# Optimization experiments

Hardware: AMD Instinct MI355X
Metric: run time of the kernel (lower is better)

Reference implementation:

```python
import jax, jax.numpy as jnp
import numpy as np

N = 1_000_000   # total atoms in batched graph
G = 50_000      # number of molecules (graphs)
F = 128         # gnn_out_feats (node feature dim)
H = 128         # classifier_hidden_feats
T = 12          # n_tasks
EPS = 1e-5      # BatchNorm1d eps


def setup_inputs() -> dict:
    key = jax.random.key(0)
    ks = jax.random.split(key, 20)
    s = 0.05
    inp = {}
    inp["node_feats"] = jax.random.normal(ks[0], (N, F), jnp.float32)
    inp["segment_ids"] = jnp.sort(jax.random.randint(ks[1], (N,), 0, G))
    inp["num_graphs"] = G
    # per-task atom weighting: Linear(F,1) per task, stacked -> [T,F]
    inp["atom_w"] = jax.random.normal(ks[2], (T, F), jnp.float32) * s
    inp["atom_b"] = jnp.zeros((T,), jnp.float32)
    # fc_layer 1: Linear(F,H) -> ReLU -> BatchNorm1d(H) (eval mode)
    inp["W1"] = jax.random.normal(ks[3], (T, F, H), jnp.float32) * s
    inp["b1"] = jnp.zeros((T, H), jnp.float32)
    inp["g1"] = jnp.ones((T, H), jnp.float32)
    inp["be1"] = jnp.zeros((T, H), jnp.float32)
    inp["rm1"] = jnp.zeros((T, H), jnp.float32)
    inp["rv1"] = jnp.ones((T, H), jnp.float32)
    # fc_layer 2 and 3: Linear(H,H) -> ReLU -> BatchNorm1d(H)
    inp["W2"] = jax.random.normal(ks[4], (T, H, H), jnp.float32) * s
    inp["b2"] = jnp.zeros((T, H), jnp.float32)
    inp["g2"] = jnp.ones((T, H), jnp.float32)
    inp["be2"] = jnp.zeros((T, H), jnp.float32)
    inp["rm2"] = jnp.zeros((T, H), jnp.float32)
    inp["rv2"] = jnp.ones((T, H), jnp.float32)
    inp["W3"] = jax.random.normal(ks[5], (T, H, H), jnp.float32) * s
    inp["b3"] = jnp.zeros((T, H), jnp.float32)
    inp["g3"] = jnp.ones((T, H), jnp.float32)
    inp["be3"] = jnp.zeros((T, H), jnp.float32)
    inp["rm3"] = jnp.zeros((T, H), jnp.float32)
    inp["rv3"] = jnp.ones((T, H), jnp.float32)
    # output_layer: Linear(H,H) -> ReLU -> Linear(H,1)
    inp["oW1"] = jax.random.normal(ks[6], (T, H, H), jnp.float32) * s
    inp["ob1"] = jnp.zeros((T, H), jnp.float32)
    inp["oW2"] = jax.random.normal(ks[7], (T, H), jnp.float32) * s
    inp["ob2"] = jnp.zeros((T,), jnp.float32)
    return inp


def _fc(x, W, b, g, be, rm, rv):
    # Linear -> ReLU -> BatchNorm1d (eval, running stats), batched over tasks t
    y = jax.nn.relu(jnp.einsum('gti,tio->gto', x, W) + b)
    return (y - rm) * (g * jax.lax.rsqrt(rv + EPS)) + be


def reference(node_feats, segment_ids, num_graphs, atom_w, atom_b,
              W1, b1, g1, be1, rm1, rv1,
              W2, b2, g2, be2, rm2, rv2,
              W3, b3, g3, be3, rm3, rv3,
              oW1, ob1, oW2, ob2):
    n_tasks = atom_w.shape[0]
    # WeightAndSum: per-task sigmoid node weights [N,T]
    w = jax.nn.sigmoid(node_feats @ atom_w.T + atom_b)
    # per-task weighted segment-sum pooling: loop over small fixed task count
    sums = [jax.ops.segment_sum(node_feats * w[:, t:t + 1], segment_ids,
                                num_segments=num_graphs)
            for t in range(n_tasks)]
    mol = jnp.stack(sums, axis=1)  # [G, T, F]
    h = _fc(mol, W1, b1, g1, be1, rm1, rv1)
    h = _fc(h, W2, b2, g2, be2, rm2, rv2)
    h = _fc(h, W3, b3, g3, be3, rm3, rv3)
    z = jax.nn.relu(jnp.einsum('gth,tho->gto', h, oW1) + ob1)
    pred = jnp.einsum('gth,th->gt', z, oW2) + ob2  # [G, T]
    return pred
```

## Files before the change

kernel.cpp:

```cpp
#include <hip/hip_runtime.h>
#include <hip/hip_bf16.h>
#include <hip/hip_fp16.h>

typedef _Float16 f16;
typedef _Float16 f16x2 __attribute__((ext_vector_type(2)));
typedef _Float16 f16x4 __attribute__((ext_vector_type(4)));
typedef _Float16 f16x8 __attribute__((ext_vector_type(8)));
typedef float f32x4 __attribute__((ext_vector_type(4)));

#define BN_EPS 1e-5f

__global__ void seg_starts_k(const int* __restrict__ seg, int N, int G, int* __restrict__ start) {
    int n = blockIdx.x * blockDim.x + threadIdx.x;
    if (n >= N) return;
    int s = seg[n];
    int p = (n == 0) ? -1 : seg[n - 1];
    for (int g = p + 1; g <= s; ++g) start[g] = n;
    if (n == N - 1) {
        for (int g = s + 1; g <= G; ++g) start[g] = N;
    }
}

__global__ void prep_k(const float* __restrict__ W1, const float* __restrict__ b1,
                       const float* __restrict__ W2, const float* __restrict__ b2,
                       const float* __restrict__ W3, const float* __restrict__ b3,
                       const float* __restrict__ oW1, const float* __restrict__ ob1,
                       const float* __restrict__ g1, const float* __restrict__ be1,
                       const float* __restrict__ rm1, const float* __restrict__ rv1,
                       const float* __restrict__ g2, const float* __restrict__ be2,
                       const float* __restrict__ rm2, const float* __restrict__ rv2,
                       const float* __restrict__ g3, const float* __restrict__ be3,
                       const float* __restrict__ rm3, const float* __restrict__ rv3,
                       f16* __restrict__ Wt, float* __restrict__ bp) {
    int T = gridDim.x;
    int t = blockIdx.x, l = blockIdx.y;
    int o = threadIdx.x;
    __shared__ float s_sh[128], c_sh[128];

    const float *W, *b, *gg = nullptr, *be = nullptr, *rm = nullptr, *rv = nullptr;
    if (l == 0)      { W = W1;  b = b1; }
    else if (l == 1) { W = W2;  b = b2;  gg = g1; be = be1; rm = rm1; rv = rv1; }
    else if (l == 2) { W = W3;  b = b3;  gg = g2; be = be2; rm = rm2; rv = rv2; }
    else             { W = oW1; b = ob1; gg = g3; be = be3; rm = rm3; rv = rv3; }

    float s = 1.f, c = 0.f;
    if (gg) {
        float sv = gg[t * 128 + o] * rsqrtf(rv[t * 128 + o] + BN_EPS);
        s = sv;
        c = be[t * 128 + o] - rm[t * 128 + o] * sv;
    }
    s_sh[o] = s;
    c_sh[o] = c;
    __syncthreads();

    const float* Wsrc = W + (size_t)t * 128 * 128;
    f16* Wdst = Wt + (((size_t)l * T + t) * 128 + o) * 128;
    float acc = b[t * 128 + o];
    for (int i = 0; i < 128; ++i) {
        float wv = Wsrc[i * 128 + o];
        Wdst[i] = (f16)(s_sh[i] * wv);
        acc += c_sh[i] * wv;
    }
    bp[((size_t)l * T + t) * 128 + o] = acc;
}

__global__ __launch_bounds__(256) void pool_k(const float* __restrict__ feats,
                                              const float* __restrict__ atom_w,
                                              const float* __restrict__ atom_b,
                                              const int* __restrict__ start,
                                              f16* __restrict__ mol, int G) {
    __shared__ f16 xs_all[4][16][128];
    __shared__ float ws_all[4][16][16];

    int wave = threadIdx.x >> 6;
    int lane = threadIdx.x & 63;
    f16 (*xs)[128] = xs_all[wave];
    float (*wsh)[16] = ws_all[wave];

    int g = blockIdx.x * 4 + wave;
    if (g >= G) return;

    int tcol = lane & 15;
    int kg = lane >> 4;

    f16x8 bfr[4];
    float ab = 0.f;
#pragma unroll
    for (int ks = 0; ks < 4; ++ks) {
        f16x8 v = {};
        if (tcol < 12) {
            const float* s = atom_w + tcol * 128 + ks * 32 + kg * 8;
#pragma unroll
            for (int j = 0; j < 8; ++j) v[j] = (f16)s[j];
        }
        bfr[ks] = v;
    }
    if (tcol < 12) ab = atom_b[tcol];

    float accx[12], accy[12];
#pragma unroll
    for (int t = 0; t < 12; ++t) { accx[t] = 0.f; accy[t] = 0.f; }

    int a0 = start[g], a1 = start[g + 1];

    for (int c0 = a0; c0 < a1; c0 += 16) {
        int cn = a1 - c0; if (cn > 16) cn = 16;
        asm volatile("s_waitcnt lgkmcnt(0)" ::: "memory");
        __builtin_amdgcn_sched_barrier(0);

#pragma unroll
        for (int it = 0; it < 8; ++it) {
            int c = (it << 6) + lane;
            int r = c >> 5, q = c & 31;
            float4 u = make_float4(0.f, 0.f, 0.f, 0.f);
            if (r < cn) u = *(const float4*)(feats + (size_t)(c0 + r) * 128 + (q << 2));
            f16x4 h;
            h[0] = (f16)u.x; h[1] = (f16)u.y; h[2] = (f16)u.z; h[3] = (f16)u.w;
            *(f16x4*)(&xs[r][(((q >> 1) ^ (r & 7)) << 3) + ((q & 1) << 2)]) = h;
        }
        asm volatile("s_waitcnt lgkmcnt(0)" ::: "memory");
        __builtin_amdgcn_sched_barrier(0);

        f32x4 pa = {0.f, 0.f, 0.f, 0.f};
#pragma unroll
        for (int ks = 0; ks < 4; ++ks) {
            f16x8 afr = *(const f16x8*)(&xs[tcol][((((ks << 2) + kg)) ^ (tcol & 7)) << 3]);
            pa = __builtin_amdgcn_mfma_f32_16x16x32_f16(afr, bfr[ks], pa, 0, 0, 0);
        }
#pragma unroll
        for (int j = 0; j < 4; ++j) {
            float w = 1.f / (1.f + __expf(-(pa[j] + ab)));
            wsh[(kg << 2) + j][tcol] = w;
        }
        asm volatile("s_waitcnt lgkmcnt(0)" ::: "memory");
        __builtin_amdgcn_sched_barrier(0);

        for (int a = 0; a < cn; ++a) {
            f16x2 x2 = *(const f16x2*)(&xs[a][(((lane >> 2) ^ (a & 7)) << 3) + ((lane & 3) << 1)]);
            float x0 = (float)x2[0], x1 = (float)x2[1];
            f32x4 w0 = *(const f32x4*)(&wsh[a][0]);
            f32x4 w1 = *(const f32x4*)(&wsh[a][4]);
            f32x4 w2 = *(const f32x4*)(&wsh[a][8]);
#pragma unroll
            for (int j = 0; j < 4; ++j) {
                accx[j] += w0[j] * x0;     accy[j] += w0[j] * x1;
                accx[4 + j] += w1[j] * x0; accy[4 + j] += w1[j] * x1;
                accx[8 + j] += w2[j] * x0; accy[8 + j] += w2[j] * x1;
            }
        }
    }

#pragma unroll
    for (int t = 0; t < 12; ++t) {
        f16x2 h;
        h[0] = (f16)accx[t];
        h[1] = (f16)accy[t];
        *(f16x2*)(mol + ((size_t)t * G + g) * 128 + 2 * lane) = h;
    }
}

__global__ __launch_bounds__(256, 2) void fc_k(const f16* __restrict__ mol,
                                               const f16* __restrict__ Wt,
                                               const float* __restrict__ bp,
                                               const float* __restrict__ oW2,
                                               const float* __restrict__ ob2,
                                               float* __restrict__ out, int G, int T) {
    __shared__ f16 A[2][64][128];
    __shared__ f16 B[128][128];

    int t = blockIdx.y;
    int g0 = blockIdx.x * 64;
    int tid = threadIdx.x;

    {
        const f16* src = mol + (size_t)t * G * 128;
#pragma unroll
        for (int k = 0; k < 4; ++k) {
            int c = tid + k * 256;
            int r = c >> 4, sl = c & 15;
            uint4 v = make_uint4(0u, 0u, 0u, 0u);
            if (g0 + r < G) v = *(const uint4*)(src + (size_t)(g0 + r) * 128 + sl * 8);
            *(uint4*)(&A[0][r][(sl ^ (r & 7)) * 8]) = v;
        }
    }
    {
        const f16* src = Wt + ((size_t)0 * T + t) * 128 * 128;
#pragma unroll
        for (int k = 0; k < 8; ++k) {
            int c = tid + k * 256;
            int r = c >> 4, sl = c & 15;
            uint4 v = *(const uint4*)(src + (size_t)r * 128 + sl * 8);
            *(uint4*)(&B[r][(sl ^ (r & 7)) * 8]) = v;
        }
    }
    __syncthreads();

    int wid = tid >> 6, lane = tid & 63;
    int lg = lane >> 4, lr = lane & 15;
    int m0 = wid * 16;
    int arow = m0 + lr;
    float pred[4] = {0.f, 0.f, 0.f, 0.f};
    int cur = 0;

    for (int l = 0; l < 4; ++l) {
        f16x8 afr[4];
#pragma unroll
        for (int ks = 0; ks < 4; ++ks) {
            int sl = (4 * ks + lg) ^ (arow & 7);
            afr[ks] = *(const f16x8*)(&A[cur][arow][sl * 8]);
        }
        const float* bias = bp + ((size_t)l * T + t) * 128;
#pragma unroll
        for (int nf = 0; nf < 8; ++nf) {
            int n = nf * 16 + lr;
            f32x4 acc = {0.f, 0.f, 0.f, 0.f};
#pragma unroll
            for (int ks = 0; ks < 4; ++ks) {
                int sl = (4 * ks + lg) ^ (n & 7);
                f16x8 bfr = *(const f16x8*)(&B[n][sl * 8]);
                acc = __builtin_amdgcn_mfma_f32_16x16x32_f16(afr[ks], bfr, acc, 0, 0, 0);
            }
            float bv = bias[n];
            if (l < 3) {
#pragma unroll
                for (int j = 0; j < 4; ++j) {
                    float y = acc[j] + bv;
                    y = y > 0.f ? y : 0.f;
                    int rr = m0 + 4 * lg + j;
                    A[cur ^ 1][rr][(((n >> 3) ^ (rr & 7)) << 3) + (n & 7)] = (f16)y;
                }
            } else {
                float w2 = oW2[t * 128 + n];
#pragma unroll
                for (int j = 0; j < 4; ++j) {
                    float z = acc[j] + bv;
                    z = z > 0.f ? z : 0.f;
                    pred[j] += z * w2;
                }
            }
        }
        __syncthreads();
        if (l < 3) {
            const f16* src = Wt + ((size_t)(l + 1) * T + t) * 128 * 128;
#pragma unroll
            for (int k = 0; k < 8; ++k) {
                int c = tid + k * 256;
                int r = c >> 4, sl = c & 15;
                uint4 v = *(const uint4*)(src + (size_t)r * 128 + sl * 8);
                *(uint4*)(&B[r][(sl ^ (r & 7)) * 8]) = v;
            }
            __syncthreads();
            cur ^= 1;
        }
    }

#pragma unroll
    for (int m = 1; m < 16; m <<= 1) {
#pragma unroll
        for (int j = 0; j < 4; ++j) pred[j] += __shfl_xor(pred[j], m, 64);
    }
    if (lr == 0) {
        float ob = ob2[t];
#pragma unroll
        for (int j = 0; j < 4; ++j) {
            int gg = g0 + m0 + 4 * lg + j;
            if (gg < G) out[(size_t)gg * T + t] = pred[j] + ob;
        }
    }
}

extern "C" void kernel_launch(void* const* d_in, const int* in_sizes, int n_in,
                              void* d_out, int out_size, void* d_ws, size_t ws_size,
                              hipStream_t stream) {
    const float* node_feats = (const float*)d_in[0];
    const int*   seg        = (const int*)d_in[1];
    const float* atom_w     = (const float*)d_in[3];
    const float* atom_b     = (const float*)d_in[4];
    const float* W1  = (const float*)d_in[5];
    const float* b1  = (const float*)d_in[6];
    const float* g1  = (const float*)d_in[7];
    const float* be1 = (const float*)d_in[8];
    const float* rm1 = (const float*)d_in[9];
    const float* rv1 = (const float*)d_in[10];
    const float* W2  = (const float*)d_in[11];
    const float* b2  = (const float*)d_in[12];
    const float* g2  = (const float*)d_in[13];
    const float* be2 = (const float*)d_in[14];
    const float* rm2 = (const float*)d_in[15];
    const float* rv2 = (const float*)d_in[16];
    const float* W3  = (const float*)d_in[17];
    const float* b3  = (const float*)d_in[18];
    const float* g3  = (const float*)d_in[19];
    const float* be3 = (const float*)d_in[20];
    const float* rm3 = (const float*)d_in[21];
    const float* rv3 = (const float*)d_in[22];
    const float* oW1 = (const float*)d_in[23];
    const float* ob1 = (const float*)d_in[24];
    const float* oW2 = (const float*)d_in[25];
    const float* ob2 = (const float*)d_in[26];

    int T = in_sizes[4];
    int F = in_sizes[3] / T;
    int N = in_sizes[0] / F;
    int G = out_size / T;

    char* ws = (char*)d_ws;
    size_t off = 0;
    int* start = (int*)ws;
    off += (((size_t)(G + 1) * 4) + 255) & ~(size_t)255;
    f16* Wt = (f16*)(ws + off);
    off += (((size_t)4 * T * 128 * 128 * 2) + 255) & ~(size_t)255;
    float* bp = (float*)(ws + off);
    off += (((size_t)4 * T * 128 * 4) + 255) & ~(size_t)255;
    f16* mol = (f16*)(ws + off);

    seg_starts_k<<<(N + 255) / 256, 256, 0, stream>>>(seg, N, G, start);
    prep_k<<<dim3(T, 4), 128, 0, stream>>>(W1, b1, W2, b2, W3, b3, oW1, ob1,
                                           g1, be1, rm1, rv1,
                                           g2, be2, rm2, rv2,
                                           g3, be3, rm3, rv3, Wt, bp);
    pool_k<<<(G + 3) / 4, 256, 0, stream>>>(node_feats, atom_w, atom_b, start, mol, G);
    fc_k<<<dim3((G + 63) / 64, T), 256, 0, stream>>>(mol, Wt, bp, oW2, ob2,
                                                     (float*)d_out, G, T);
}
```

Measured before the change: 402.1 us.

## Pool with MFMA weighted sum, register prefetch double-buffer, and graph-major mol layout

Replaces the scalar per-atom FMA loop in the pooling kernel with a 16x16x16 f16 MFMA that multiplies the sigmoid weights (transposed, masked per atom) by the staged feature tile, removing the wsh shared buffer. Node features for the next 16-atom chunk are prefetched into registers while the current chunk is processed, and LDS is double-buffered so the explicit waitcnt barriers can be dropped. The mol intermediate switches from task-major to graph-major [G,T,F] layout, and fc_k's loads are updated to match. The risks are weights rounded to fp16, strided 2-byte scalar LDS gathers when building the B fragment, and more register pressure.

```diff
diff --git a/kernel.cpp b/kernel.cpp
--- a/kernel.cpp
+++ b/kernel.cpp
@@ -69,18 +69,16 @@
                                               const float* __restrict__ atom_b,
                                               const int* __restrict__ start,
                                               f16* __restrict__ mol, int G) {
-    __shared__ f16 xs_all[4][16][128];
-    __shared__ float ws_all[4][16][16];
+    __shared__ f16 xs_all[4][2][16][128];
 
     int wave = threadIdx.x >> 6;
     int lane = threadIdx.x & 63;
-    f16 (*xs)[128] = xs_all[wave];
-    float (*wsh)[16] = ws_all[wave];
+    f16 (*xs)[16][128] = xs_all[wave];
 
     int g = blockIdx.x * 4 + wave;
     if (g >= G) return;
 
-    int tcol = lane & 15;
+    int lr = lane & 15;
     int kg = lane >> 4;
 
     f16x8 bfr[4];
@@ -88,74 +86,96 @@
 #pragma unroll
     for (int ks = 0; ks < 4; ++ks) {
         f16x8 v = {};
-        if (tcol < 12) {
-            const float* s = atom_w + tcol * 128 + ks * 32 + kg * 8;
+        if (lr < 12) {
+            const float* s = atom_w + lr * 128 + ks * 32 + kg * 8;
 #pragma unroll
             for (int j = 0; j < 8; ++j) v[j] = (f16)s[j];
         }
         bfr[ks] = v;
     }
-    if (tcol < 12) ab = atom_b[tcol];
-
-    float accx[12], accy[12];
-#pragma unroll
-    for (int t = 0; t < 12; ++t) { accx[t] = 0.f; accy[t] = 0.f; }
+    if (lr < 12) ab = atom_b[lr];
+
+    f32x4 acc[8];
+#pragma unroll
+    for (int nf = 0; nf < 8; ++nf) acc[nf] = (f32x4){0.f, 0.f, 0.f, 0.f};
 
     int a0 = start[g], a1 = start[g + 1];
-
-    for (int c0 = a0; c0 < a1; c0 += 16) {
-        int cn = a1 - c0; if (cn > 16) cn = 16;
-        asm volatile("s_waitcnt lgkmcnt(0)" ::: "memory");
-        __builtin_amdgcn_sched_barrier(0);
-
+    int nAtoms = a1 - a0;
+    int nc = (nAtoms + 15) >> 4;
+
+    float4 u[8];
+    if (nc > 0) {
+        int cn = nAtoms < 16 ? nAtoms : 16;
 #pragma unroll
         for (int it = 0; it < 8; ++it) {
             int c = (it << 6) + lane;
             int r = c >> 5, q = c & 31;
-            float4 u = make_float4(0.f, 0.f, 0.f, 0.f);
-            if (r < cn) u = *(const float4*)(feats + (size_t)(c0 + r) * 128 + (q << 2));
+            float4 v = make_float4(0.f, 0.f, 0.f, 0.f);
+            if (r < cn) v = *(const float4*)(feats + (size_t)(a0 + r) * 128 + (q << 2));
+            u[it] = v;
+        }
+    }
+
+    for (int ci = 0; ci < nc; ++ci) {
+        int cur = ci & 1;
+#pragma unroll
+        for (int it = 0; it < 8; ++it) {
+            int c = (it << 6) + lane;
+            int r = c >> 5, q = c & 31;
             f16x4 h;
-            h[0] = (f16)u.x; h[1] = (f16)u.y; h[2] = (f16)u.z; h[3] = (f16)u.w;
-            *(f16x4*)(&xs[r][(((q >> 1) ^ (r & 7)) << 3) + ((q & 1) << 2)]) = h;
-        }
-        asm volatile("s_waitcnt lgkmcnt(0)" ::: "memory");
-        __builtin_amdgcn_sched_barrier(0);
+            h[0] = (f16)u[it].x; h[1] = (f16)u[it].y;
+            h[2] = (f16)u[it].z; h[3] = (f16)u[it].w;
+            *(f16x4*)(&xs[cur][r][(((q >> 1) ^ (r & 7)) << 3) + ((q & 1) << 2)]) = h;
+        }
+        if (ci + 1 < nc) {
+            int c0 = a0 + (ci + 1) * 16;
+            int cn2 = a1 - c0; if (cn2 > 16) cn2 = 16;
+#pragma unroll
+            for (int it = 0; it < 8; ++it) {
+                int c = (it << 6) + lane;
+                int r = c >> 5, q = c & 31;
+                float4 v = make_float4(0.f, 0.f, 0.f, 0.f);
+                if (r < cn2) v = *(const float4*)(feats + (size_t)(c0 + r) * 128 + (q << 2));
+                u[it] = v;
+            }
+        }
+        int cn = nAtoms - ci * 16; if (cn > 16) cn = 16;
 
         f32x4 pa = {0.f, 0.f, 0.f, 0.f};
 #pragma unroll
         for (int ks = 0; ks < 4; ++ks) {
-            f16x8 afr = *(const f16x8*)(&xs[tcol][((((ks << 2) + kg)) ^ (tcol & 7)) << 3]);
+            f16x8 afr = *(const f16x8*)(&xs[cur][lr][((((ks << 2) + kg)) ^ (lr & 7)) << 3]);
             pa = __builtin_amdgcn_mfma_f32_16x16x32_f16(afr, bfr[ks], pa, 0, 0, 0);
         }
+        f16x4 a2;
 #pragma unroll
         for (int j = 0; j < 4; ++j) {
             float w = 1.f / (1.f + __expf(-(pa[j] + ab)));
-            wsh[(kg << 2) + j][tcol] = w;
-        }
-        asm volatile("s_waitcnt lgkmcnt(0)" ::: "memory");
-        __builtin_amdgcn_sched_barrier(0);
-
-        for (int a = 0; a < cn; ++a) {
-            f16x2 x2 = *(const f16x2*)(&xs[a][(((lane >> 2) ^ (a & 7)) << 3) + ((lane & 3) << 1)]);
-            float x0 = (float)x2[0], x1 = (float)x2[1];
-            f32x4 w0 = *(const f32x4*)(&wsh[a][0]);
-            f32x4 w1 = *(const f32x4*)(&wsh[a][4]);
-            f32x4 w2 = *(const f32x4*)(&wsh[a][8]);
+            int atom = (kg << 2) + j;
+            a2[j] = (atom < cn) ? (f16)w : (f16)0.f;
+        }
+#pragma unroll
+        for (int nf = 0; nf < 8; ++nf) {
+            f16x4 b2;
 #pragma unroll
             for (int j = 0; j < 4; ++j) {
-                accx[j] += w0[j] * x0;     accy[j] += w0[j] * x1;
-                accx[4 + j] += w1[j] * x0; accy[4 + j] += w1[j] * x1;
-                accx[8 + j] += w2[j] * x0; accy[8 + j] += w2[j] * x1;
-            }
-        }
-    }
-
-#pragma unroll
-    for (int t = 0; t < 12; ++t) {
-        f16x2 h;
-        h[0] = (f16)accx[t];
-        h[1] = (f16)accy[t];
-        *(f16x2*)(mol + ((size_t)t * G + g) * 128 + 2 * lane) = h;
+                int a = (kg << 2) + j;
+                int f = (nf << 4) + lr;
+                b2[j] = xs[cur][a][(((f >> 3) ^ (a & 7)) << 3) + (f & 7)];
+            }
+            acc[nf] = __builtin_amdgcn_mfma_f32_16x16x16f16(a2, b2, acc[nf], 0, 0, 0);
+        }
+    }
+
+    f16* dst = mol + (size_t)g * 12 * 128;
+    if (kg < 3) {
+#pragma unroll
+        for (int nf = 0; nf < 8; ++nf) {
+#pragma unroll
+            for (int j = 0; j < 4; ++j) {
+                dst[((kg << 2) + j) * 128 + (nf << 4) + lr] = (f16)acc[nf][j];
+            }
+        }
     }
 }
 
@@ -173,13 +193,13 @@
     int tid = threadIdx.x;
 
     {
-        const f16* src = mol + (size_t)t * G * 128;
 #pragma unroll
         for (int k = 0; k < 4; ++k) {
             int c = tid + k * 256;
             int r = c >> 4, sl = c & 15;
             uint4 v = make_uint4(0u, 0u, 0u, 0u);
-            if (g0 + r < G) v = *(const uint4*)(src + (size_t)(g0 + r) * 128 + sl * 8);
+            if (g0 + r < G)
+                v = *(const uint4*)(mol + ((size_t)(g0 + r) * T + t) * 128 + sl * 8);
             *(uint4*)(&A[0][r][(sl ^ (r & 7)) * 8]) = v;
         }
     }
```

Result: faster. 372.6 us (-7.3%).
